# Kernel optimization log

Hardware: AMD Instinct MI355X
Metric: run time of the kernel (lower is better)

Reference implementation:

```python
import jax, jax.numpy as jnp
import numpy as np

B, N, C, G = 32, 1024, 64, 64

def setup_inputs() -> dict:
    key = jax.random.key(0)
    ks = jax.random.split(key, 8)
    return {
        "x": jax.random.normal(ks[0], (B, N, C), dtype=jnp.float32),
        "valid_len": jax.random.randint(ks[1], (B,), 0, N, dtype=jnp.int64) if jax.config.jax_enable_x64 else jax.random.randint(ks[1], (B,), 0, N, dtype=jnp.int32),
        "Wq": jax.random.normal(ks[2], (C, G), dtype=jnp.float32) * 0.1,
        "bq": jax.random.normal(ks[3], (G,), dtype=jnp.float32) * 0.1,
        "Wk": jax.random.normal(ks[4], (C, G), dtype=jnp.float32) * 0.1,
        "bk": jax.random.normal(ks[5], (G,), dtype=jnp.float32) * 0.1,
        "Wv": jax.random.normal(ks[6], (C, G), dtype=jnp.float32) * 0.1,
        "bv": jax.random.normal(ks[7], (G,), dtype=jnp.float32) * 0.1,
    }

def reference(x, valid_len, Wq, bq, Wk, bk, Wv, bv):
    # x: [B, N, C]; valid_len: [B] int (number of valid key positions per batch)
    q = x @ Wq + bq                                   # [B, N, G]
    k = x @ Wk + bk                                   # [B, N, G]
    v = x @ Wv + bv                                   # [B, N, G]
    scores = jnp.einsum('bnd,bmd->bnm', q, k)         # [B, N, N] (no 1/sqrt(d) scale)
    # mask: key positions >= valid_len[b] get -1e6 (matches original's -1000000.0 fill)
    col = jnp.arange(scores.shape[-1])
    mask = col[None, None, :] >= valid_len[:, None, None]
    scores = jnp.where(mask, jnp.float32(-1000000.0), scores)
    attn = jax.nn.softmax(scores, axis=-1)            # [B, N, N]
    return jnp.einsum('bnm,bmd->bnd', attn, v)        # [B, N, G]
```

## Files before the change

### kernel.cpp

```cpp
#include <hip/hip_runtime.h>
#include <stdint.h>


typedef __attribute__((ext_vector_type(4))) float    floatx4;
typedef __attribute__((ext_vector_type(8))) _Float16 halfx8;

static __device__ __forceinline__ unsigned short f2h(float f) {
    union { _Float16 h; unsigned short u; } v; v.h = (_Float16)f;
    return v.u;
}
static __device__ __forceinline__ float h2f(unsigned short u) {
    union { unsigned short u; _Float16 h; } v; v.u = u;
    return (float)v.h;
}

__global__ __launch_bounds__(256) void qkv_proj_kernel(
    const float* __restrict__ x,
    const float* __restrict__ Wq, const float* __restrict__ bq,
    const float* __restrict__ Wk, const float* __restrict__ bk,
    const float* __restrict__ Wv, const float* __restrict__ bv,
    unsigned short* __restrict__ q_ws, unsigned short* __restrict__ k_ws,
    unsigned short* __restrict__ vt_ws)
{
    __shared__ __align__(16) unsigned short smem[8 * 4096];
    float* vtmp = (float*)&smem[2 * 4096];

    const int XS_HI = 0, XS_LO = 4096;
    #define WT_OFF(i) (2 * 4096 + (i) * 4096)

    const int tid  = threadIdx.x;
    const int blk  = blockIdx.x;
    const int row0 = blk * 64;
    const int b    = blk >> 4;
    const int n0   = (blk & 15) * 64;
    const int lane = tid & 63;
    const int w    = tid >> 6;
    const int l15  = lane & 15;
    const int quad = lane >> 4;

#pragma unroll
    for (int i = 0; i < 2; ++i) {
        int id = i * 256 + tid;
        int r = id >> 3, c8 = id & 7;
        const float4* gp = (const float4*)(x + (row0 + r) * 64 + c8 * 8);
        float4 f0 = gp[0], f1 = gp[1];
        float fv[8] = { f0.x, f0.y, f0.z, f0.w, f1.x, f1.y, f1.z, f1.w };
        __align__(16) unsigned short thi[8], tlo[8];
#pragma unroll
        for (int j = 0; j < 8; ++j) {
            unsigned short hi = f2h(fv[j]);
            thi[j] = hi;
            tlo[j] = f2h(fv[j] - h2f(hi));
        }
        int idx = r * 64 + ((c8 ^ (r & 7)) * 8);
        *(uint4*)&smem[XS_HI + idx] = *(uint4*)thi;
        *(uint4*)&smem[XS_LO + idx] = *(uint4*)tlo;
    }
    {
        const float* Ws[3] = { Wq, Wk, Wv };
        int g = tid & 63, ci = tid >> 6;
#pragma unroll
        for (int wi = 0; wi < 3; ++wi) {
#pragma unroll
            for (int j = 0; j < 16; ++j) {
                int c = ci * 16 + j;
                float f = Ws[wi][c * 64 + g];
                unsigned short hi = f2h(f);
                unsigned short lo = f2h(f - h2f(hi));
                int c8 = c >> 3;
                int idx = g * 64 + ((c8 ^ (g & 7)) * 8) + (c & 7);
                smem[WT_OFF(wi * 2 + 0) + idx] = hi;
                smem[WT_OFF(wi * 2 + 1) + idx] = lo;
            }
        }
    }
    __syncthreads();

    const int arow = w * 16 + l15;
    const int aidx0 = arow * 64 + (((0 + quad) ^ (arow & 7)) * 8);
    const int aidx1 = arow * 64 + (((4 + quad) ^ (arow & 7)) * 8);
    halfx8 a_hi0 = *(const halfx8*)&smem[XS_HI + aidx0];
    halfx8 a_hi1 = *(const halfx8*)&smem[XS_HI + aidx1];
    halfx8 a_lo0 = *(const halfx8*)&smem[XS_LO + aidx0];
    halfx8 a_lo1 = *(const halfx8*)&smem[XS_LO + aidx1];

    __syncthreads();

    unsigned short* q_lds = &smem[0];
    unsigned short* k_lds = &smem[4096];

    const float* biases[3] = { bq, bk, bv };
    floatx4 vacc[4];
#pragma unroll
    for (int wi = 0; wi < 3; ++wi) {
#pragma unroll
        for (int gs = 0; gs < 4; ++gs) {
            int g0 = gs * 16;
            float bias = biases[wi][g0 + l15];
            floatx4 acc = { bias, bias, bias, bias };
            int brow = g0 + l15;
            int bidx0 = brow * 64 + (((0 + quad) ^ (brow & 7)) * 8);
            int bidx1 = brow * 64 + (((4 + quad) ^ (brow & 7)) * 8);
            halfx8 b_hi0 = *(const halfx8*)&smem[WT_OFF(wi * 2 + 0) + bidx0];
            halfx8 b_hi1 = *(const halfx8*)&smem[WT_OFF(wi * 2 + 0) + bidx1];
            halfx8 b_lo0 = *(const halfx8*)&smem[WT_OFF(wi * 2 + 1) + bidx0];
            halfx8 b_lo1 = *(const halfx8*)&smem[WT_OFF(wi * 2 + 1) + bidx1];
            acc = __builtin_amdgcn_mfma_f32_16x16x32_f16(a_hi0, b_hi0, acc, 0, 0, 0);
            acc = __builtin_amdgcn_mfma_f32_16x16x32_f16(a_hi1, b_hi1, acc, 0, 0, 0);
            acc = __builtin_amdgcn_mfma_f32_16x16x32_f16(a_hi0, b_lo0, acc, 0, 0, 0);
            acc = __builtin_amdgcn_mfma_f32_16x16x32_f16(a_hi1, b_lo1, acc, 0, 0, 0);
            acc = __builtin_amdgcn_mfma_f32_16x16x32_f16(a_lo0, b_hi0, acc, 0, 0, 0);
            acc = __builtin_amdgcn_mfma_f32_16x16x32_f16(a_lo1, b_hi1, acc, 0, 0, 0);
            if (wi < 2) {
                unsigned short* dst = (wi == 0) ? q_lds : k_lds;
                int c8 = gs * 2 + (l15 >> 3);
#pragma unroll
                for (int r = 0; r < 4; ++r) {
                    int row = w * 16 + quad * 4 + r;
                    dst[row * 64 + ((c8 ^ (row & 7)) * 8) + (l15 & 7)] = f2h(acc[r]);
                }
            } else {
                vacc[gs] = acc;
            }
        }
    }

    __syncthreads();

#pragma unroll
    for (int i = 0; i < 2; ++i) {
        int id = i * 256 + tid;
        int r = id >> 3, c8 = id & 7;
        int sidx = r * 64 + ((c8 ^ (r & 7)) * 8);
        *(uint4*)(q_ws + (row0 + r) * 64 + c8 * 8) = *(const uint4*)&q_lds[sidx];
        *(uint4*)(k_ws + (row0 + r) * 64 + c8 * 8) = *(const uint4*)&k_lds[sidx];
    }

#pragma unroll
    for (int gs = 0; gs < 4; ++gs) {
#pragma unroll
        for (int r = 0; r < 4; ++r) {
            int nl = w * 16 + quad * 4 + r;
            vtmp[(gs * 16 + l15) * 65 + nl] = vacc[gs][r];
        }
    }
    __syncthreads();
    {
        int g = tid >> 2, c4 = tid & 3;
        __align__(16) unsigned short tmp[16];
#pragma unroll
        for (int j = 0; j < 16; ++j) tmp[j] = f2h(vtmp[g * 65 + c4 * 16 + j]);
        unsigned short* dst = vt_ws + (b * 64 + g) * 1024 + n0 + c4 * 16;
        *(uint4*)(dst)     = ((uint4*)tmp)[0];
        *(uint4*)(dst + 8) = ((uint4*)tmp)[1];
    }
    #undef WT_OFF
}

__global__ __launch_bounds__(256) void attn_kernel(
    const unsigned short* __restrict__ q_ws, const unsigned short* __restrict__ k_ws,
    const unsigned short* __restrict__ vt_ws, const int* __restrict__ valid_len,
    float* __restrict__ out)
{
    __shared__ __align__(16) unsigned short qs[4096];
    __shared__ __align__(16) unsigned short kbuf[2][4096];
    __shared__ __align__(16) unsigned short vbuf[2][4096];
    __shared__ __align__(16) unsigned short ps[4 * 1024];

    const int tid  = threadIdx.x;
    const int blk  = blockIdx.x;
    const int b    = blk >> 4;
    const int row0 = blk * 64;
    const int lane = tid & 63;
    const int w    = tid >> 6;
    const int l15  = lane & 15;
    const int quad = lane >> 4;

    const int r_a  = tid >> 3,          c8_a = tid & 7;
    const int r_b  = (256 + tid) >> 3,  c8_b = tid & 7;
    const int lidx_a = r_a * 64 + ((c8_a ^ (r_a & 7)) * 8);
    const int lidx_b = r_b * 64 + ((c8_b ^ (r_b & 7)) * 8);

    *(uint4*)&qs[lidx_a] = *(const uint4*)(q_ws + (row0 + r_a) * 64 + c8_a * 8);
    *(uint4*)&qs[lidx_b] = *(const uint4*)(q_ws + (row0 + r_b) * 64 + c8_b * 8);

    const int vl    = valid_len[b];
    const float mv  = (vl > 0) ? -1000000.0f : 0.0f;
    const int nt    = (vl == 0) ? 16 : ((vl + 63) >> 6);
    const int fullt = vl >> 6;

    const unsigned short* kbase = k_ws + (size_t)b * 1024 * 64;
    const unsigned short* vbase = vt_ws + (size_t)b * 64 * 1024;

    uint4 kr0 = *(const uint4*)(kbase + r_a * 64 + c8_a * 8);
    uint4 kr1 = *(const uint4*)(kbase + r_b * 64 + c8_b * 8);
    *(uint4*)&kbuf[0][lidx_a] = kr0;
    *(uint4*)&kbuf[0][lidx_b] = kr1;

    __syncthreads();

    const int arow = w * 16 + l15;
    halfx8 aq0 = *(const halfx8*)&qs[arow * 64 + (((0 + quad) ^ (arow & 7)) * 8)];
    halfx8 aq1 = *(const halfx8*)&qs[arow * 64 + (((4 + quad) ^ (arow & 7)) * 8)];

    float m_lane[4] = { -1000000.0f, -1000000.0f, -1000000.0f, -1000000.0f };
    for (int t = 0; t < nt; ++t) {
        bool pre = (t + 1) < nt;
        if (pre) {
            const unsigned short* kp = kbase + (t + 1) * 64 * 64;
            kr0 = *(const uint4*)(kp + r_a * 64 + c8_a * 8);
            kr1 = *(const uint4*)(kp + r_b * 64 + c8_b * 8);
        }
        __syncthreads();
        if (pre) {
            *(uint4*)&kbuf[(t + 1) & 1][lidx_a] = kr0;
            *(uint4*)&kbuf[(t + 1) & 1][lidx_b] = kr1;
        }
        const unsigned short* ksb = kbuf[t & 1];

        floatx4 s[4];
#pragma unroll
        for (int sub = 0; sub < 4; ++sub) {
            int krow = sub * 16 + l15;
            halfx8 bk0 = *(const halfx8*)&ksb[krow * 64 + (((0 + quad) ^ (krow & 7)) * 8)];
            halfx8 bk1 = *(const halfx8*)&ksb[krow * 64 + (((4 + quad) ^ (krow & 7)) * 8)];
            floatx4 acc = { 0, 0, 0, 0 };
            acc = __builtin_amdgcn_mfma_f32_16x16x32_f16(aq0, bk0, acc, 0, 0, 0);
            acc = __builtin_amdgcn_mfma_f32_16x16x32_f16(aq1, bk1, acc, 0, 0, 0);
            s[sub] = acc;
        }
        if (t >= fullt) {
#pragma unroll
            for (int sub = 0; sub < 4; ++sub) {
                int key = t * 64 + sub * 16 + l15;
                if (key >= vl) { s[sub][0] = mv; s[sub][1] = mv; s[sub][2] = mv; s[sub][3] = mv; }
            }
        }
#pragma unroll
        for (int r = 0; r < 4; ++r)
            m_lane[r] = fmaxf(m_lane[r],
                        fmaxf(fmaxf(s[0][r], s[1][r]), fmaxf(s[2][r], s[3][r])));
    }

    float m[4];
#pragma unroll
    for (int r = 0; r < 4; ++r) {
        float mm = m_lane[r];
#pragma unroll
        for (int off = 1; off < 16; off <<= 1)
            mm = fmaxf(mm, __shfl_xor(mm, off, 64));
        m[r] = mm;
    }

    kr0 = *(const uint4*)(kbase + r_a * 64 + c8_a * 8);
    kr1 = *(const uint4*)(kbase + r_b * 64 + c8_b * 8);
    uint4 vr0 = *(const uint4*)(vbase + r_a * 1024 + c8_a * 8);
    uint4 vr1 = *(const uint4*)(vbase + r_b * 1024 + c8_b * 8);
    __syncthreads();
    *(uint4*)&kbuf[0][lidx_a] = kr0;
    *(uint4*)&kbuf[0][lidx_b] = kr1;
    *(uint4*)&vbuf[0][lidx_a] = vr0;
    *(uint4*)&vbuf[0][lidx_b] = vr1;

    float l_lane[4] = { 0.f, 0.f, 0.f, 0.f };
    floatx4 o[4] = { {0,0,0,0}, {0,0,0,0}, {0,0,0,0}, {0,0,0,0} };

    for (int t = 0; t < nt; ++t) {
        bool pre = (t + 1) < nt;
        if (pre) {
            const unsigned short* kp = kbase + (t + 1) * 64 * 64;
            const unsigned short* vp = vbase + (t + 1) * 64;
            kr0 = *(const uint4*)(kp + r_a * 64 + c8_a * 8);
            kr1 = *(const uint4*)(kp + r_b * 64 + c8_b * 8);
            vr0 = *(const uint4*)(vp + r_a * 1024 + c8_a * 8);
            vr1 = *(const uint4*)(vp + r_b * 1024 + c8_b * 8);
        }
        __syncthreads();
        if (pre) {
            *(uint4*)&kbuf[(t + 1) & 1][lidx_a] = kr0;
            *(uint4*)&kbuf[(t + 1) & 1][lidx_b] = kr1;
            *(uint4*)&vbuf[(t + 1) & 1][lidx_a] = vr0;
            *(uint4*)&vbuf[(t + 1) & 1][lidx_b] = vr1;
        }
        const unsigned short* ksb = kbuf[t & 1];
        const unsigned short* vsb = vbuf[t & 1];

        floatx4 s[4];
#pragma unroll
        for (int sub = 0; sub < 4; ++sub) {
            int krow = sub * 16 + l15;
            halfx8 bk0 = *(const halfx8*)&ksb[krow * 64 + (((0 + quad) ^ (krow & 7)) * 8)];
            halfx8 bk1 = *(const halfx8*)&ksb[krow * 64 + (((4 + quad) ^ (krow & 7)) * 8)];
            floatx4 acc = { 0, 0, 0, 0 };
            acc = __builtin_amdgcn_mfma_f32_16x16x32_f16(aq0, bk0, acc, 0, 0, 0);
            acc = __builtin_amdgcn_mfma_f32_16x16x32_f16(aq1, bk1, acc, 0, 0, 0);
            s[sub] = acc;
        }
        if (t >= fullt) {
#pragma unroll
            for (int sub = 0; sub < 4; ++sub) {
                int key = t * 64 + sub * 16 + l15;
                if (key >= vl) { s[sub][0] = mv; s[sub][1] = mv; s[sub][2] = mv; s[sub][3] = mv; }
            }
        }

        unsigned short* psw = &ps[w * 1024];
#pragma unroll
        for (int sub = 0; sub < 4; ++sub) {
            int c8 = sub * 2 + (l15 >> 3);
#pragma unroll
            for (int r = 0; r < 4; ++r) {
                float p = __expf(s[sub][r] - m[r]);
                l_lane[r] += p;
                int row = quad * 4 + r;
                psw[row * 64 + ((c8 ^ (row & 7)) * 8) + (l15 & 7)] = f2h(p);
            }
        }
        halfx8 ap0 = *(const halfx8*)&psw[l15 * 64 + (((0 + quad) ^ (l15 & 7)) * 8)];
        halfx8 ap1 = *(const halfx8*)&psw[l15 * 64 + (((4 + quad) ^ (l15 & 7)) * 8)];

#pragma unroll
        for (int gs = 0; gs < 4; ++gs) {
            int grow = gs * 16 + l15;
            halfx8 bv0 = *(const halfx8*)&vsb[grow * 64 + (((0 + quad) ^ (grow & 7)) * 8)];
            halfx8 bv1 = *(const halfx8*)&vsb[grow * 64 + (((4 + quad) ^ (grow & 7)) * 8)];
            o[gs] = __builtin_amdgcn_mfma_f32_16x16x32_f16(ap0, bv0, o[gs], 0, 0, 0);
            o[gs] = __builtin_amdgcn_mfma_f32_16x16x32_f16(ap1, bv1, o[gs], 0, 0, 0);
        }
    }

    float l[4];
#pragma unroll
    for (int r = 0; r < 4; ++r) {
        float ss = l_lane[r];
#pragma unroll
        for (int off = 1; off < 16; off <<= 1)
            ss += __shfl_xor(ss, off, 64);
        l[r] = ss;
    }
#pragma unroll
    for (int gs = 0; gs < 4; ++gs) {
#pragma unroll
        for (int r = 0; r < 4; ++r) {
            int row = row0 + w * 16 + quad * 4 + r;
            out[row * 64 + gs * 16 + l15] = o[gs][r] / l[r];
        }
    }
}

extern "C" void kernel_launch(void* const* d_in, const int* in_sizes, int n_in,
                              void* d_out, int out_size, void* d_ws, size_t ws_size,
                              hipStream_t stream) {
    const float* x    = (const float*)d_in[0];
    const int*   vlen = (const int*)  d_in[1];
    const float* Wq   = (const float*)d_in[2];
    const float* bq   = (const float*)d_in[3];
    const float* Wk   = (const float*)d_in[4];
    const float* bk   = (const float*)d_in[5];
    const float* Wv   = (const float*)d_in[6];
    const float* bv   = (const float*)d_in[7];
    float* out = (float*)d_out;

    unsigned short* q_ws  = (unsigned short*)d_ws;
    unsigned short* k_ws  = q_ws + 32768 * 64;
    unsigned short* vt_ws = k_ws + 32768 * 64;

    qkv_proj_kernel<<<512, 256, 0, stream>>>(x, Wq, bq, Wk, bk, Wv, bv, q_ws, k_ws, vt_ws);
    attn_kernel<<<512, 256, 0, stream>>>(q_ws, k_ws, vt_ws, vlen, out);
}
```

Measured before the change: 106.8 us.

## Use online softmax in attention and pre-pack split-fp16 weights in separate kernel

The attention kernel replaces its two-pass scheme (a max pass over all K tiles, then an exp/PV pass) with a single-pass online softmax. It keeps a running max per row and rescales the accumulator and row sums by alpha each tile, so K is read once instead of twice. A small prep kernel converts Wq/Wk/Wv once into swizzled hi/lo fp16 planes, so each of the 512 projection blocks no longer repeats that conversion and just copies the packed planes into LDS. The cost is an extra kernel launch plus per-tile shuffle reductions and rescales in the attention loop. The masked fill for empty rows changes from 0 to -1e6, which still gives a uniform distribution.

```diff
diff --git a/kernel.cpp b/kernel.cpp
--- a/kernel.cpp
+++ b/kernel.cpp
@@ -14,11 +14,30 @@
     return (float)v.h;
 }
 
+__global__ __launch_bounds__(256) void wprep_kernel(
+    const float* __restrict__ Wq, const float* __restrict__ Wk,
+    const float* __restrict__ Wv, unsigned short* __restrict__ wt_pack)
+{
+    const int plane = blockIdx.x;
+    const int wi = plane >> 1, hl = plane & 1;
+    const float* W = (wi == 0) ? Wq : (wi == 1) ? Wk : Wv;
+    const int tid = threadIdx.x;
+    const int g = tid & 63, cb = (tid >> 6) * 16;
+#pragma unroll
+    for (int j = 0; j < 16; ++j) {
+        int c = cb + j;
+        float f = W[c * 64 + g];
+        unsigned short hi = f2h(f);
+        unsigned short v = hl ? f2h(f - h2f(hi)) : hi;
+        int idx = g * 64 + ((((c >> 3) ^ (g & 7))) * 8) + (c & 7);
+        wt_pack[plane * 4096 + idx] = v;
+    }
+}
+
 __global__ __launch_bounds__(256) void qkv_proj_kernel(
     const float* __restrict__ x,
-    const float* __restrict__ Wq, const float* __restrict__ bq,
-    const float* __restrict__ Wk, const float* __restrict__ bk,
-    const float* __restrict__ Wv, const float* __restrict__ bv,
+    const unsigned short* __restrict__ wt_pack,
+    const float* __restrict__ bq, const float* __restrict__ bk, const float* __restrict__ bv,
     unsigned short* __restrict__ q_ws, unsigned short* __restrict__ k_ws,
     unsigned short* __restrict__ vt_ws)
 {
@@ -39,6 +58,16 @@
     const int quad = lane >> 4;
 
 #pragma unroll
+    for (int i = 0; i < 6; ++i) {
+#pragma unroll
+        for (int pp = 0; pp < 2; ++pp) {
+            int e = (pp * 256 + tid) * 8;
+            *(uint4*)&smem[2 * 4096 + i * 4096 + e] =
+                *(const uint4*)&wt_pack[i * 4096 + e];
+        }
+    }
+
+#pragma unroll
     for (int i = 0; i < 2; ++i) {
         int id = i * 256 + tid;
         int r = id >> 3, c8 = id & 7;
@@ -55,24 +84,6 @@
         int idx = r * 64 + ((c8 ^ (r & 7)) * 8);
         *(uint4*)&smem[XS_HI + idx] = *(uint4*)thi;
         *(uint4*)&smem[XS_LO + idx] = *(uint4*)tlo;
-    }
-    {
-        const float* Ws[3] = { Wq, Wk, Wv };
-        int g = tid & 63, ci = tid >> 6;
-#pragma unroll
-        for (int wi = 0; wi < 3; ++wi) {
-#pragma unroll
-            for (int j = 0; j < 16; ++j) {
-                int c = ci * 16 + j;
-                float f = Ws[wi][c * 64 + g];
-                unsigned short hi = f2h(f);
-                unsigned short lo = f2h(f - h2f(hi));
-                int c8 = c >> 3;
-                int idx = g * 64 + ((c8 ^ (g & 7)) * 8) + (c & 7);
-                smem[WT_OFF(wi * 2 + 0) + idx] = hi;
-                smem[WT_OFF(wi * 2 + 1) + idx] = lo;
-            }
-        }
     }
     __syncthreads();
 
@@ -185,7 +196,6 @@
     *(uint4*)&qs[lidx_b] = *(const uint4*)(q_ws + (row0 + r_b) * 64 + c8_b * 8);
 
     const int vl    = valid_len[b];
-    const float mv  = (vl > 0) ? -1000000.0f : 0.0f;
     const int nt    = (vl == 0) ? 16 : ((vl + 63) >> 6);
     const int fullt = vl >> 6;
 
@@ -194,74 +204,20 @@
 
     uint4 kr0 = *(const uint4*)(kbase + r_a * 64 + c8_a * 8);
     uint4 kr1 = *(const uint4*)(kbase + r_b * 64 + c8_b * 8);
-    *(uint4*)&kbuf[0][lidx_a] = kr0;
-    *(uint4*)&kbuf[0][lidx_b] = kr1;
-
-    __syncthreads();
-
-    const int arow = w * 16 + l15;
-    halfx8 aq0 = *(const halfx8*)&qs[arow * 64 + (((0 + quad) ^ (arow & 7)) * 8)];
-    halfx8 aq1 = *(const halfx8*)&qs[arow * 64 + (((4 + quad) ^ (arow & 7)) * 8)];
-
-    float m_lane[4] = { -1000000.0f, -1000000.0f, -1000000.0f, -1000000.0f };
-    for (int t = 0; t < nt; ++t) {
-        bool pre = (t + 1) < nt;
-        if (pre) {
-            const unsigned short* kp = kbase + (t + 1) * 64 * 64;
-            kr0 = *(const uint4*)(kp + r_a * 64 + c8_a * 8);
-            kr1 = *(const uint4*)(kp + r_b * 64 + c8_b * 8);
-        }
-        __syncthreads();
-        if (pre) {
-            *(uint4*)&kbuf[(t + 1) & 1][lidx_a] = kr0;
-            *(uint4*)&kbuf[(t + 1) & 1][lidx_b] = kr1;
-        }
-        const unsigned short* ksb = kbuf[t & 1];
-
-        floatx4 s[4];
-#pragma unroll
-        for (int sub = 0; sub < 4; ++sub) {
-            int krow = sub * 16 + l15;
-            halfx8 bk0 = *(const halfx8*)&ksb[krow * 64 + (((0 + quad) ^ (krow & 7)) * 8)];
-            halfx8 bk1 = *(const halfx8*)&ksb[krow * 64 + (((4 + quad) ^ (krow & 7)) * 8)];
-            floatx4 acc = { 0, 0, 0, 0 };
-            acc = __builtin_amdgcn_mfma_f32_16x16x32_f16(aq0, bk0, acc, 0, 0, 0);
-            acc = __builtin_amdgcn_mfma_f32_16x16x32_f16(aq1, bk1, acc, 0, 0, 0);
-            s[sub] = acc;
-        }
-        if (t >= fullt) {
-#pragma unroll
-            for (int sub = 0; sub < 4; ++sub) {
-                int key = t * 64 + sub * 16 + l15;
-                if (key >= vl) { s[sub][0] = mv; s[sub][1] = mv; s[sub][2] = mv; s[sub][3] = mv; }
-            }
-        }
-#pragma unroll
-        for (int r = 0; r < 4; ++r)
-            m_lane[r] = fmaxf(m_lane[r],
-                        fmaxf(fmaxf(s[0][r], s[1][r]), fmaxf(s[2][r], s[3][r])));
-    }
-
-    float m[4];
-#pragma unroll
-    for (int r = 0; r < 4; ++r) {
-        float mm = m_lane[r];
-#pragma unroll
-        for (int off = 1; off < 16; off <<= 1)
-            mm = fmaxf(mm, __shfl_xor(mm, off, 64));
-        m[r] = mm;
-    }
-
-    kr0 = *(const uint4*)(kbase + r_a * 64 + c8_a * 8);
-    kr1 = *(const uint4*)(kbase + r_b * 64 + c8_b * 8);
     uint4 vr0 = *(const uint4*)(vbase + r_a * 1024 + c8_a * 8);
     uint4 vr1 = *(const uint4*)(vbase + r_b * 1024 + c8_b * 8);
-    __syncthreads();
     *(uint4*)&kbuf[0][lidx_a] = kr0;
     *(uint4*)&kbuf[0][lidx_b] = kr1;
     *(uint4*)&vbuf[0][lidx_a] = vr0;
     *(uint4*)&vbuf[0][lidx_b] = vr1;
 
+    __syncthreads();
+
+    const int arow = w * 16 + l15;
+    halfx8 aq0 = *(const halfx8*)&qs[arow * 64 + (((0 + quad) ^ (arow & 7)) * 8)];
+    halfx8 aq1 = *(const halfx8*)&qs[arow * 64 + (((4 + quad) ^ (arow & 7)) * 8)];
+
+    float m_r[4]    = { -INFINITY, -INFINITY, -INFINITY, -INFINITY };
     float l_lane[4] = { 0.f, 0.f, 0.f, 0.f };
     floatx4 o[4] = { {0,0,0,0}, {0,0,0,0}, {0,0,0,0}, {0,0,0,0} };
 
@@ -275,7 +231,7 @@
             vr0 = *(const uint4*)(vp + r_a * 1024 + c8_a * 8);
             vr1 = *(const uint4*)(vp + r_b * 1024 + c8_b * 8);
         }
-        __syncthreads();
+        if (t > 0) __syncthreads();
         if (pre) {
             *(uint4*)&kbuf[(t + 1) & 1][lidx_a] = kr0;
             *(uint4*)&kbuf[(t + 1) & 1][lidx_b] = kr1;
@@ -300,8 +256,34 @@
 #pragma unroll
             for (int sub = 0; sub < 4; ++sub) {
                 int key = t * 64 + sub * 16 + l15;
-                if (key >= vl) { s[sub][0] = mv; s[sub][1] = mv; s[sub][2] = mv; s[sub][3] = mv; }
+                if (key >= vl) { s[sub][0] = -1e6f; s[sub][1] = -1e6f; s[sub][2] = -1e6f; s[sub][3] = -1e6f; }
             }
+        }
+
+        float p[4][4];
+        float alpha[4];
+#pragma unroll
+        for (int r = 0; r < 4; ++r) {
+            float mx = fmaxf(fmaxf(s[0][r], s[1][r]), fmaxf(s[2][r], s[3][r]));
+#pragma unroll
+            for (int off = 1; off < 16; off <<= 1)
+                mx = fmaxf(mx, __shfl_xor(mx, off, 64));
+            float mnew = fmaxf(m_r[r], mx);
+            alpha[r] = __expf(m_r[r] - mnew);
+            float psum = 0.f;
+#pragma unroll
+            for (int sub = 0; sub < 4; ++sub) {
+                float pv = __expf(s[sub][r] - mnew);
+                p[sub][r] = pv;
+                psum += pv;
+            }
+            l_lane[r] = l_lane[r] * alpha[r] + psum;
+            m_r[r] = mnew;
+        }
+#pragma unroll
+        for (int gs = 0; gs < 4; ++gs) {
+            o[gs][0] *= alpha[0]; o[gs][1] *= alpha[1];
+            o[gs][2] *= alpha[2]; o[gs][3] *= alpha[3];
         }
 
         unsigned short* psw = &ps[w * 1024];
@@ -310,10 +292,8 @@
             int c8 = sub * 2 + (l15 >> 3);
 #pragma unroll
             for (int r = 0; r < 4; ++r) {
-                float p = __expf(s[sub][r] - m[r]);
-                l_lane[r] += p;
                 int row = quad * 4 + r;
-                psw[row * 64 + ((c8 ^ (row & 7)) * 8) + (l15 & 7)] = f2h(p);
+                psw[row * 64 + ((c8 ^ (row & 7)) * 8) + (l15 & 7)] = f2h(p[sub][r]);
             }
         }
         halfx8 ap0 = *(const halfx8*)&psw[l15 * 64 + (((0 + quad) ^ (l15 & 7)) * 8)];
@@ -361,10 +341,12 @@
     const float* bv   = (const float*)d_in[7];
     float* out = (float*)d_out;
 
-    unsigned short* q_ws  = (unsigned short*)d_ws;
-    unsigned short* k_ws  = q_ws + 32768 * 64;
-    unsigned short* vt_ws = k_ws + 32768 * 64;
-
-    qkv_proj_kernel<<<512, 256, 0, stream>>>(x, Wq, bq, Wk, bk, Wv, bv, q_ws, k_ws, vt_ws);
+    unsigned short* q_ws    = (unsigned short*)d_ws;
+    unsigned short* k_ws    = q_ws + 32768 * 64;
+    unsigned short* vt_ws   = k_ws + 32768 * 64;
+    unsigned short* wt_pack = vt_ws + 32 * 64 * 1024;
+
+    wprep_kernel<<<6, 256, 0, stream>>>(Wq, Wk, Wv, wt_pack);
+    qkv_proj_kernel<<<512, 256, 0, stream>>>(x, wt_pack, bq, bk, bv, q_ws, k_ws, vt_ws);
     attn_kernel<<<512, 256, 0, stream>>>(q_ws, k_ws, vt_ws, vlen, out);
 }
```

After: 107.8 us. Within noise of the previous version (+0.9%).
